# Kernel optimization log

Hardware: AMD Instinct MI355X
Metric: run time of the kernel (lower is better)

## Reference

```python
import jax, jax.numpy as jnp
import numpy as np

B, Q, K, H = 8, 512, 512, 1024
NH, HD = 16, 64
MAX_REL = 512  # max_relative_positions


def setup_inputs() -> dict:
    key = jax.random.key(0)
    ks = jax.random.split(key, 16)
    s = 1.0 / np.sqrt(H)
    inp = {
        "query": jax.random.normal(ks[0], (B, Q, H), jnp.float32),
        "key": jax.random.normal(ks[1], (B, K, H), jnp.float32),
        "value": jax.random.normal(ks[2], (B, K, H), jnp.float32),
        "key_padding_mask": jax.random.randint(ks[3], (B, K), 0, 2, jnp.int32),
        "Wq": jax.random.normal(ks[4], (H, H), jnp.float32) * s,
        "bq": jnp.zeros((H,), jnp.float32),
        "Wk": jax.random.normal(ks[5], (H, H), jnp.float32) * s,
        "bk": jnp.zeros((H,), jnp.float32),
        "Wv": jax.random.normal(ks[6], (H, H), jnp.float32) * s,
        "bv": jnp.zeros((H,), jnp.float32),
        "Wo": jax.random.normal(ks[7], (H, H), jnp.float32) * s,
        "bo": jnp.zeros((H,), jnp.float32),
        "rel_table": jax.random.normal(ks[8], (2 * MAX_REL - 1, NH), jnp.float32) * 0.02,
        "local_bias": jax.random.normal(ks[9], (512, 512), jnp.float32) * 0.1,
        "log_scale": jnp.zeros((1,), jnp.float32),
        "attention_bias": jnp.zeros((1,), jnp.float32),
    }
    return inp


def reference(query, key, value, key_padding_mask, Wq, bq, Wk, bk, Wv, bv, Wo, bo,
              rel_table, local_bias, log_scale, attention_bias):
    # projections -> [B, NH, len, HD]
    q = (query @ Wq + bq).reshape(B, Q, NH, HD).transpose(0, 2, 1, 3)
    k = (key @ Wk + bk).reshape(B, K, NH, HD).transpose(0, 2, 1, 3)
    v = (value @ Wv + bv).reshape(B, K, NH, HD).transpose(0, 2, 1, 3)

    scores = jnp.einsum('bhqd,bhkd->bhqk', q, k) / jnp.sqrt(jnp.float32(HD))

    # relative position bias
    rel = jnp.arange(Q)[:, None] - jnp.arange(K)[None, :]
    bucket = jnp.clip(rel, -(MAX_REL - 1), MAX_REL - 1) + (MAX_REL - 1)
    rel_bias = rel_table[bucket]            # [Q, K, NH]
    scores = scores + rel_bias.transpose(2, 0, 1)[None]  # [1, NH, Q, K]

    # local bias (Q,K <= 512)
    scores = scores + local_bias[:Q, :K][None, None] * 0.05

    scale = jnp.clip(jnp.exp(log_scale), 1.0, 4.0)
    scores = scores * scale + attention_bias

    pad = (key_padding_mask == 0)[:, None, None, :]  # [B,1,1,K]
    scores = jnp.where(pad, -jnp.inf, scores)
    # clamp AFTER masking: -inf -> -50 (padded keys get tiny but nonzero weight)
    scores = jnp.clip(scores, -50.0, 50.0)

    attn = jax.nn.softmax(scores, axis=-1)
    out = jnp.einsum('bhqk,bhkd->bhqd', attn, v)
    out = out.transpose(0, 2, 1, 3).reshape(B, Q, H)
    out = out @ Wo + bo
    return out, attn
```

## Files before the change

### kernel.cpp

```cpp
#include <hip/hip_runtime.h>

#define B_ 8
#define LQ 512
#define LK 512
#define HDIM 1024
#define NH_ 16
#define HD_ 64

typedef unsigned short u16;
typedef __attribute__((ext_vector_type(4))) float f32x4;
typedef __attribute__((ext_vector_type(4))) int i32x4;
typedef __attribute__((ext_vector_type(8))) __bf16 bf16x8;

static __device__ __forceinline__ u16 f2bf(float f) {
    union { float f; unsigned u; } v; v.f = f;
    unsigned u = v.u;
    return (u16)((u + 0x7fffu + ((u >> 16) & 1u)) >> 16);
}

static __device__ __forceinline__ void gload_lds16(const u16* g, u16* l) {
    __builtin_amdgcn_global_load_lds((const __attribute__((address_space(1))) unsigned*)g,
                                     (__attribute__((address_space(3))) unsigned*)l, 16, 0, 0);
}

__global__ __launch_bounds__(256) void xcast_kernel(
    const float* __restrict__ x0, const float* __restrict__ x1, const float* __restrict__ x2,
    u16* __restrict__ o0, u16* __restrict__ o1, u16* __restrict__ o2)
{
    const float* X; u16* O;
    switch (blockIdx.z) { case 0: X = x0; O = o0; break; case 1: X = x1; O = o1; break;
                          default: X = x2; O = o2; }
    int i = blockIdx.x * 256 + threadIdx.x;
    f32x4 v = ((const f32x4*)X)[i];
    union { u16 u[4]; unsigned long long ull; } p;
    p.u[0] = f2bf(v[0]); p.u[1] = f2bf(v[1]); p.u[2] = f2bf(v[2]); p.u[3] = f2bf(v[3]);
    ((unsigned long long*)O)[i] = p.ull;
}

__global__ void wcast_kernel(const float* __restrict__ w0, const float* __restrict__ w1,
                             const float* __restrict__ w2, const float* __restrict__ w3,
                             u16* __restrict__ o0, u16* __restrict__ o1,
                             u16* __restrict__ o2, u16* __restrict__ o3) {
    const float* W; u16* O;
    switch (blockIdx.z) { case 0: W = w0; O = o0; break; case 1: W = w1; O = o1; break;
                          case 2: W = w2; O = o2; break; default: W = w3; O = o3; }
    __shared__ float t[32][33];
    int tx = threadIdx.x, ty = threadIdx.y;
    int n0 = blockIdx.x * 32, k0 = blockIdx.y * 32;
#pragma unroll
    for (int i = 0; i < 4; i++) {
        int k = ty * 4 + i;
        t[k][tx] = W[(k0 + k) * HDIM + n0 + tx];
    }
    __syncthreads();
#pragma unroll
    for (int i = 0; i < 4; i++) {
        int n = ty * 4 + i;
        O[(n0 + n) * HDIM + k0 + tx] = f2bf(t[tx][n]);
    }
}

__global__ __launch_bounds__(256) void proj2_kernel(
    const u16* __restrict__ x0, const u16* __restrict__ x1, const u16* __restrict__ x2,
    const u16* __restrict__ wt0, const u16* __restrict__ wt1, const u16* __restrict__ wt2,
    const float* __restrict__ bi0, const float* __restrict__ bi1, const float* __restrict__ bi2,
    u16* __restrict__ ot0, u16* __restrict__ ot1, u16* __restrict__ ot2)
{
    __shared__ u16 As[128 * 64];
    __shared__ u16 Bs[128 * 64];
    int bid = blockIdx.x;
    int swz = (bid & 7) * 96 + (bid >> 3);
    int z = swz >> 8, rem = swz & 255;
    int Mb = (rem >> 3) * 128, Nb = (rem & 7) * 128;
    const u16* X; const u16* WT; const float* bias; u16* out;
    switch (z) {
        case 0: X = x0; WT = wt0; bias = bi0; out = ot0; break;
        case 1: X = x1; WT = wt1; bias = bi1; out = ot1; break;
        default: X = x2; WT = wt2; bias = bi2; out = ot2; break;
    }
    int tid = threadIdx.x, lane = tid & 63, w = tid >> 6;
    int wm = (w & 1) * 64, wn = (w >> 1) * 64;
    int r16 = lane & 15, kg = lane >> 4;
    int rsw = (r16 & 7) * 8;
    int srow = lane >> 3;
    int scol = 8 * ((lane & 7) ^ (lane >> 3));
    const u16* gA = X + (size_t)Mb * HDIM;
    const u16* gB = WT + (size_t)Nb * HDIM;

    f32x4 acc[4][4] = {};
    for (int k0 = 0; k0 < HDIM; k0 += 64) {
#pragma unroll
        for (int i = 0; i < 4; i++) {
            int c = w * 4 + i;
            int row = c * 8 + srow;
            gload_lds16(&gA[(size_t)row * HDIM + k0 + scol], &As[c * 512]);
            gload_lds16(&gB[(size_t)row * HDIM + k0 + scol], &Bs[c * 512]);
        }
        __syncthreads();
#pragma unroll
        for (int kk = 0; kk < 2; kk++) {
            int colp = (kk * 32 + kg * 8) ^ rsw;
            bf16x8 a[4], b[4];
#pragma unroll
            for (int mt = 0; mt < 4; mt++) a[mt] = *(const bf16x8*)&As[(wm + mt * 16 + r16) * 64 + colp];
#pragma unroll
            for (int nt = 0; nt < 4; nt++) b[nt] = *(const bf16x8*)&Bs[(wn + nt * 16 + r16) * 64 + colp];
#pragma unroll
            for (int mt = 0; mt < 4; mt++)
#pragma unroll
                for (int nt = 0; nt < 4; nt++)
                    acc[mt][nt] = __builtin_amdgcn_mfma_f32_16x16x32_bf16(a[mt], b[nt], acc[mt][nt], 0, 0, 0);
        }
        __syncthreads();
    }
    int cr = (lane >> 4) * 4, cc = lane & 15;
#pragma unroll
    for (int nt = 0; nt < 4; nt++) {
        int n = Nb + wn + nt * 16 + cc;
        float bv = bias[n];
        int h = n >> 6, d = n & 63;
#pragma unroll
        for (int mt = 0; mt < 4; mt++) {
#pragma unroll
            for (int j = 0; j < 4; j++) {
                int m = Mb + wm + mt * 16 + cr + j;
                int b = m >> 9, l = m & 511;
                out[(((b * NH_ + h) * LQ) + l) * HD_ + d] = f2bf(acc[mt][nt][j] + bv);
            }
        }
    }
}

__global__ void vtrans_kernel(const u16* __restrict__ vb, u16* __restrict__ vT) {
    int bh = blockIdx.z;
    int k0 = blockIdx.x * 32, d0 = blockIdx.y * 32;
    __shared__ u16 t[32][33];
    int tx = threadIdx.x, ty = threadIdx.y;
    const u16* src = vb + (size_t)bh * (LK * HD_);
    u16* dst = vT + (size_t)bh * (LK * HD_);
#pragma unroll
    for (int i = 0; i < 4; i++) {
        int k = ty * 4 + i;
        t[k][tx] = src[(k0 + k) * HD_ + d0 + tx];
    }
    __syncthreads();
#pragma unroll
    for (int i = 0; i < 4; i++) {
        int d = ty * 4 + i;
        dst[(d0 + d) * LK + k0 + tx] = t[tx][d];
    }
}

__global__ __launch_bounds__(512) void scores_kernel(
    const u16* __restrict__ qb, const u16* __restrict__ kb,
    const int* __restrict__ kpm, const float* __restrict__ rel_table,
    const float* __restrict__ local_bias, const float* __restrict__ log_scale,
    const float* __restrict__ att_bias, float* __restrict__ attn_out)
{
    __shared__ u16 Qs[32][72];
    __shared__ float rel_l[1024];
    __shared__ int pmask[512];
    __shared__ float red[2][32][8];

    int bh = blockIdx.y;
    int q0 = blockIdx.x * 32;
    int b = bh >> 4, h = bh & 15;
    int tid = threadIdx.x, lane = tid & 63, w = tid >> 6;
    int r16 = lane & 15, kg = lane >> 4;

    float scale = fminf(fmaxf(__expf(log_scale[0]), 1.0f), 4.0f);
    float abias = att_bias[0];

    if (tid < 256) {
        int row = tid >> 3, c8 = tid & 7;
        *(i32x4*)&Qs[row][c8 * 8] = *(const i32x4*)&qb[((size_t)bh * LQ + q0 + row) * HD_ + c8 * 8];
    }
    for (int i = tid; i < 1023; i += 512) rel_l[i] = rel_table[i * NH_ + h];
    pmask[tid & 511] = kpm[b * LK + (tid & 511)];
    __syncthreads();

    bf16x8 aq[2][2];
#pragma unroll
    for (int m = 0; m < 2; m++)
#pragma unroll
        for (int kk = 0; kk < 2; kk++)
            aq[m][kk] = *(const bf16x8*)&Qs[m * 16 + r16][kk * 32 + kg * 8];

    f32x4 acc[2][4] = {};
    const u16* kbase = kb + ((size_t)bh * LK + w * 64) * HD_;
#pragma unroll
    for (int nt = 0; nt < 4; nt++) {
        bf16x8 bk0 = *(const bf16x8*)&kbase[(nt * 16 + r16) * HD_ + kg * 8];
        bf16x8 bk1 = *(const bf16x8*)&kbase[(nt * 16 + r16) * HD_ + 32 + kg * 8];
#pragma unroll
        for (int m = 0; m < 2; m++) {
            acc[m][nt] = __builtin_amdgcn_mfma_f32_16x16x32_bf16(aq[m][0], bk0, acc[m][nt], 0, 0, 0);
            acc[m][nt] = __builtin_amdgcn_mfma_f32_16x16x32_bf16(aq[m][1], bk1, acc[m][nt], 0, 0, 0);
        }
    }

    float rm[2][4];
#pragma unroll
    for (int m = 0; m < 2; m++)
#pragma unroll
        for (int j = 0; j < 4; j++) rm[m][j] = -1e30f;
#pragma unroll
    for (int m = 0; m < 2; m++) {
#pragma unroll
        for (int nt = 0; nt < 4; nt++) {
            int ki = w * 64 + nt * 16 + r16;
            bool masked = (pmask[ki] == 0);
#pragma unroll
            for (int j = 0; j < 4; j++) {
                int row = m * 16 + kg * 4 + j;
                int qi = q0 + row;
                float s = acc[m][nt][j] * 0.125f;
                s += rel_l[qi - ki + 511];
                s += local_bias[qi * LK + ki] * 0.05f;
                s = s * scale + abias;
                s = masked ? -50.0f : fminf(fmaxf(s, -50.0f), 50.0f);
                acc[m][nt][j] = s;
                rm[m][j] = fmaxf(rm[m][j], s);
            }
        }
    }
#pragma unroll
    for (int m = 0; m < 2; m++)
#pragma unroll
        for (int j = 0; j < 4; j++) {
            float v = rm[m][j];
            v = fmaxf(v, __shfl_xor(v, 1));
            v = fmaxf(v, __shfl_xor(v, 2));
            v = fmaxf(v, __shfl_xor(v, 4));
            v = fmaxf(v, __shfl_xor(v, 8));
            rm[m][j] = v;
        }
    if (r16 == 0) {
#pragma unroll
        for (int m = 0; m < 2; m++)
#pragma unroll
            for (int j = 0; j < 4; j++) red[0][m * 16 + kg * 4 + j][w] = rm[m][j];
    }
    __syncthreads();
    float fm[2][4];
#pragma unroll
    for (int m = 0; m < 2; m++)
#pragma unroll
        for (int j = 0; j < 4; j++) {
            int row = m * 16 + kg * 4 + j;
            float v = red[0][row][0];
#pragma unroll
            for (int ww = 1; ww < 8; ww++) v = fmaxf(v, red[0][row][ww]);
            fm[m][j] = v;
        }
    float ps[2][4] = {};
#pragma unroll
    for (int m = 0; m < 2; m++)
#pragma unroll
        for (int nt = 0; nt < 4; nt++)
#pragma unroll
            for (int j = 0; j < 4; j++) {
                float e = __expf(acc[m][nt][j] - fm[m][j]);
                acc[m][nt][j] = e;
                ps[m][j] += e;
            }
#pragma unroll
    for (int m = 0; m < 2; m++)
#pragma unroll
        for (int j = 0; j < 4; j++) {
            float v = ps[m][j];
            v += __shfl_xor(v, 1);
            v += __shfl_xor(v, 2);
            v += __shfl_xor(v, 4);
            v += __shfl_xor(v, 8);
            ps[m][j] = v;
        }
    if (r16 == 0) {
#pragma unroll
        for (int m = 0; m < 2; m++)
#pragma unroll
            for (int j = 0; j < 4; j++) red[1][m * 16 + kg * 4 + j][w] = ps[m][j];
    }
    __syncthreads();
    float* dst = attn_out + ((size_t)bh * LQ + q0) * (size_t)LK + w * 64;
#pragma unroll
    for (int m = 0; m < 2; m++)
#pragma unroll
        for (int j = 0; j < 4; j++) {
            int row = m * 16 + kg * 4 + j;
            float sum = 0.f;
#pragma unroll
            for (int ww = 0; ww < 8; ww++) sum += red[1][row][ww];
            float inv = 1.0f / sum;
#pragma unroll
            for (int nt = 0; nt < 4; nt++)
                dst[(size_t)row * LK + nt * 16 + r16] = acc[m][nt][j] * inv;
        }
}

__global__ __launch_bounds__(256) void pv_kernel(
    const float* __restrict__ attn, const u16* __restrict__ vT, u16* __restrict__ ctx)
{
    __shared__ u16 As[128][72];
    __shared__ u16 Bs[64][72];
    int bh = blockIdx.y;
    int b = bh >> 4, h = bh & 15;
    int Mb = blockIdx.x * 128;
    int tid = threadIdx.x, lane = tid & 63, wid = tid >> 6;
    int wm = wid >> 1, wn = wid & 1;
    int r16 = lane & 15, kg = lane >> 4;
    f32x4 acc[4][2] = {};
    const float* abase = attn + ((size_t)bh * LQ + Mb) * (size_t)LK;
    const u16* vbase = vT + (size_t)bh * (HD_ * LK);
    for (int kt = 0; kt < 8; kt++) {
#pragma unroll
        for (int i = 0; i < 8; i++) {
            int g = tid + i * 256;
            int row = g >> 4, c4 = g & 15;
            f32x4 av = *(const f32x4*)&abase[(size_t)row * LK + kt * 64 + c4 * 4];
            union { u16 u[4]; unsigned long long ull; } p;
            p.u[0] = f2bf(av[0]); p.u[1] = f2bf(av[1]);
            p.u[2] = f2bf(av[2]); p.u[3] = f2bf(av[3]);
            *(unsigned long long*)&As[row][c4 * 4] = p.ull;
        }
#pragma unroll
        for (int i = 0; i < 2; i++) {
            int g = tid + i * 256;
            int row = g >> 3, c8 = g & 7;
            *(i32x4*)&Bs[row][c8 * 8] = *(const i32x4*)&vbase[(size_t)row * LK + kt * 64 + c8 * 8];
        }
        __syncthreads();
#pragma unroll
        for (int kk = 0; kk < 2; kk++) {
            bf16x8 a[4], bfr[2];
#pragma unroll
            for (int mt = 0; mt < 4; mt++) a[mt] = *(const bf16x8*)&As[wm * 64 + mt * 16 + r16][kk * 32 + kg * 8];
#pragma unroll
            for (int nt = 0; nt < 2; nt++) bfr[nt] = *(const bf16x8*)&Bs[wn * 32 + nt * 16 + r16][kk * 32 + kg * 8];
#pragma unroll
            for (int mt = 0; mt < 4; mt++)
#pragma unroll
                for (int nt = 0; nt < 2; nt++)
                    acc[mt][nt] = __builtin_amdgcn_mfma_f32_16x16x32_bf16(a[mt], bfr[nt], acc[mt][nt], 0, 0, 0);
        }
        __syncthreads();
    }
    int cr = (lane >> 4) * 4, cc = lane & 15;
#pragma unroll
    for (int mt = 0; mt < 4; mt++) {
#pragma unroll
        for (int nt = 0; nt < 2; nt++) {
            int d = wn * 32 + nt * 16 + cc;
#pragma unroll
            for (int j = 0; j < 4; j++) {
                int q = Mb + wm * 64 + mt * 16 + cr + j;
                ctx[((size_t)(b * LQ + q)) * HDIM + h * HD_ + d] = f2bf(acc[mt][nt][j]);
            }
        }
    }
}

__global__ __launch_bounds__(256) void oproj2_kernel(
    const u16* __restrict__ ctx, const u16* __restrict__ WT,
    const float* __restrict__ bias, float* __restrict__ out)
{
    __shared__ u16 As[128 * 64];
    __shared__ u16 Bs[128 * 64];
    int bid = blockIdx.x;
    int idx = (bid & 7) * 32 + (bid >> 3);
    int Mb = (idx >> 3) * 128, Nb = (idx & 7) * 128;
    int tid = threadIdx.x, lane = tid & 63, w = tid >> 6;
    int wm = (w & 1) * 64, wn = (w >> 1) * 64;
    int r16 = lane & 15, kg = lane >> 4;
    int rsw = (r16 & 7) * 8;
    int srow = lane >> 3;
    int scol = 8 * ((lane & 7) ^ (lane >> 3));
    const u16* gA = ctx + (size_t)Mb * HDIM;
    const u16* gB = WT + (size_t)Nb * HDIM;

    f32x4 acc[4][4] = {};
    for (int k0 = 0; k0 < HDIM; k0 += 64) {
#pragma unroll
        for (int i = 0; i < 4; i++) {
            int c = w * 4 + i;
            int row = c * 8 + srow;
            gload_lds16(&gA[(size_t)row * HDIM + k0 + scol], &As[c * 512]);
            gload_lds16(&gB[(size_t)row * HDIM + k0 + scol], &Bs[c * 512]);
        }
        __syncthreads();
#pragma unroll
        for (int kk = 0; kk < 2; kk++) {
            int colp = (kk * 32 + kg * 8) ^ rsw;
            bf16x8 a[4], b[4];
#pragma unroll
            for (int mt = 0; mt < 4; mt++) a[mt] = *(const bf16x8*)&As[(wm + mt * 16 + r16) * 64 + colp];
#pragma unroll
            for (int nt = 0; nt < 4; nt++) b[nt] = *(const bf16x8*)&Bs[(wn + nt * 16 + r16) * 64 + colp];
#pragma unroll
            for (int mt = 0; mt < 4; mt++)
#pragma unroll
                for (int nt = 0; nt < 4; nt++)
                    acc[mt][nt] = __builtin_amdgcn_mfma_f32_16x16x32_bf16(a[mt], b[nt], acc[mt][nt], 0, 0, 0);
        }
        __syncthreads();
    }
    int cr = (lane >> 4) * 4, cc = lane & 15;
#pragma unroll
    for (int nt = 0; nt < 4; nt++) {
        int n = Nb + wn + nt * 16 + cc;
        float bv = bias[n];
#pragma unroll
        for (int mt = 0; mt < 4; mt++) {
#pragma unroll
            for (int j = 0; j < 4; j++) {
                int m = Mb + wm + mt * 16 + cr + j;
                out[(size_t)m * HDIM + n] = acc[mt][nt][j] + bv;
            }
        }
    }
}

extern "C" void kernel_launch(void* const* d_in, const int* in_sizes, int n_in,
                              void* d_out, int out_size, void* d_ws, size_t ws_size,
                              hipStream_t stream) {
    (void)in_sizes; (void)n_in; (void)out_size; (void)ws_size;
    const float* query = (const float*)d_in[0];
    const float* key_  = (const float*)d_in[1];
    const float* value = (const float*)d_in[2];
    const int*   kpm   = (const int*)d_in[3];
    const float* Wq = (const float*)d_in[4];  const float* bq = (const float*)d_in[5];
    const float* Wk = (const float*)d_in[6];  const float* bk = (const float*)d_in[7];
    const float* Wv = (const float*)d_in[8];  const float* bv = (const float*)d_in[9];
    const float* Wo = (const float*)d_in[10]; const float* bo = (const float*)d_in[11];
    const float* rel_table  = (const float*)d_in[12];
    const float* local_bias = (const float*)d_in[13];
    const float* log_scale  = (const float*)d_in[14];
    const float* att_bias   = (const float*)d_in[15];

    char* ws = (char*)d_ws;
    u16* WTq = (u16*)(ws + 0ull);
    u16* WTk = (u16*)(ws + (2ull << 20));
    u16* WTv = (u16*)(ws + (4ull << 20));
    u16* WTo = (u16*)(ws + (6ull << 20));
    u16* qb  = (u16*)(ws + (8ull << 20));
    u16* kb  = (u16*)(ws + (16ull << 20));
    u16* vb  = (u16*)(ws + (24ull << 20));
    u16* vT  = (u16*)(ws + (32ull << 20));
    u16* ctx = (u16*)(ws + (40ull << 20));
    u16* xq  = (u16*)(ws + (32ull << 20));
    u16* xk  = (u16*)(ws + (40ull << 20));
    u16* xv  = (u16*)(ws + (48ull << 20));

    float* out  = (float*)d_out;
    float* attn = out + (size_t)4096 * 1024;

    xcast_kernel<<<dim3(4096, 1, 3), 256, 0, stream>>>(query, key_, value, xq, xk, xv);
    wcast_kernel<<<dim3(32, 32, 4), dim3(32, 8), 0, stream>>>(Wq, Wk, Wv, Wo, WTq, WTk, WTv, WTo);
    proj2_kernel<<<768, 256, 0, stream>>>(xq, xk, xv, WTq, WTk, WTv, bq, bk, bv, qb, kb, vb);
    vtrans_kernel<<<dim3(16, 2, 128), dim3(32, 8), 0, stream>>>(vb, vT);
    scores_kernel<<<dim3(16, 128), 512, 0, stream>>>(qb, kb, kpm, rel_table, local_bias,
                                                     log_scale, att_bias, attn);
    pv_kernel<<<dim3(4, 128), 256, 0, stream>>>(attn, vT, ctx);
    oproj2_kernel<<<256, 256, 0, stream>>>(ctx, WTo, bo, out);
}
```

Measured before the change: 196.9 us.

## Fuse P·V into scores kernel using bf16 probabilities kept in LDS

Merges the separate pv_kernel into the scores/softmax kernel. Normalized probabilities are written to the fp32 attn output and also stored as bf16 in shared memory, then multiplied by V directly (V fragments read from global), with the two K-halves split across warps and reduced through LDS. This removes re-reading the 64 MB fp32 attention matrix and a kernel launch. The cost is about 36 KB of extra LDS per block, which may lower occupancy, and uncached global V fragment loads per warp.

```diff
diff --git a/kernel.cpp b/kernel.cpp
--- a/kernel.cpp
+++ b/kernel.cpp
@@ -151,16 +151,18 @@
     }
 }
 
-__global__ __launch_bounds__(512) void scores_kernel(
-    const u16* __restrict__ qb, const u16* __restrict__ kb,
+__global__ __launch_bounds__(512) void attn2_kernel(
+    const u16* __restrict__ qb, const u16* __restrict__ kb, const u16* __restrict__ vT,
     const int* __restrict__ kpm, const float* __restrict__ rel_table,
     const float* __restrict__ local_bias, const float* __restrict__ log_scale,
-    const float* __restrict__ att_bias, float* __restrict__ attn_out)
+    const float* __restrict__ att_bias, float* __restrict__ attn_out, u16* __restrict__ ctx)
 {
     __shared__ u16 Qs[32][72];
     __shared__ float rel_l[1024];
     __shared__ int pmask[512];
     __shared__ float red[2][32][8];
+    __shared__ u16 P[32][520];
+    __shared__ float pred[4][32][16];
 
     int bh = blockIdx.y;
     int q0 = blockIdx.x * 32;
@@ -282,6 +284,7 @@
             for (int j = 0; j < 4; j++) red[1][m * 16 + kg * 4 + j][w] = ps[m][j];
     }
     __syncthreads();
+
     float* dst = attn_out + ((size_t)bh * LQ + q0) * (size_t)LK + w * 64;
 #pragma unroll
     for (int m = 0; m < 2; m++)
@@ -293,70 +296,45 @@
             for (int ww = 0; ww < 8; ww++) sum += red[1][row][ww];
             float inv = 1.0f / sum;
 #pragma unroll
-            for (int nt = 0; nt < 4; nt++)
-                dst[(size_t)row * LK + nt * 16 + r16] = acc[m][nt][j] * inv;
-        }
-}
-
-__global__ __launch_bounds__(256) void pv_kernel(
-    const float* __restrict__ attn, const u16* __restrict__ vT, u16* __restrict__ ctx)
-{
-    __shared__ u16 As[128][72];
-    __shared__ u16 Bs[64][72];
-    int bh = blockIdx.y;
-    int b = bh >> 4, h = bh & 15;
-    int Mb = blockIdx.x * 128;
-    int tid = threadIdx.x, lane = tid & 63, wid = tid >> 6;
-    int wm = wid >> 1, wn = wid & 1;
-    int r16 = lane & 15, kg = lane >> 4;
-    f32x4 acc[4][2] = {};
-    const float* abase = attn + ((size_t)bh * LQ + Mb) * (size_t)LK;
+            for (int nt = 0; nt < 4; nt++) {
+                float p = acc[m][nt][j] * inv;
+                dst[(size_t)row * LK + nt * 16 + r16] = p;
+                P[row][w * 64 + nt * 16 + r16] = f2bf(p);
+            }
+        }
+    __syncthreads();
+
+    int wd = (w & 3) * 16;
+    int kh = (w >> 2) * 256;
     const u16* vbase = vT + (size_t)bh * (HD_ * LK);
+    f32x4 po[2] = {};
+#pragma unroll
     for (int kt = 0; kt < 8; kt++) {
-#pragma unroll
-        for (int i = 0; i < 8; i++) {
-            int g = tid + i * 256;
-            int row = g >> 4, c4 = g & 15;
-            f32x4 av = *(const f32x4*)&abase[(size_t)row * LK + kt * 64 + c4 * 4];
-            union { u16 u[4]; unsigned long long ull; } p;
-            p.u[0] = f2bf(av[0]); p.u[1] = f2bf(av[1]);
-            p.u[2] = f2bf(av[2]); p.u[3] = f2bf(av[3]);
-            *(unsigned long long*)&As[row][c4 * 4] = p.ull;
-        }
-#pragma unroll
-        for (int i = 0; i < 2; i++) {
-            int g = tid + i * 256;
-            int row = g >> 3, c8 = g & 7;
-            *(i32x4*)&Bs[row][c8 * 8] = *(const i32x4*)&vbase[(size_t)row * LK + kt * 64 + c8 * 8];
-        }
-        __syncthreads();
-#pragma unroll
-        for (int kk = 0; kk < 2; kk++) {
-            bf16x8 a[4], bfr[2];
-#pragma unroll
-            for (int mt = 0; mt < 4; mt++) a[mt] = *(const bf16x8*)&As[wm * 64 + mt * 16 + r16][kk * 32 + kg * 8];
-#pragma unroll
-            for (int nt = 0; nt < 2; nt++) bfr[nt] = *(const bf16x8*)&Bs[wn * 32 + nt * 16 + r16][kk * 32 + kg * 8];
-#pragma unroll
-            for (int mt = 0; mt < 4; mt++)
-#pragma unroll
-                for (int nt = 0; nt < 2; nt++)
-                    acc[mt][nt] = __builtin_amdgcn_mfma_f32_16x16x32_bf16(a[mt], bfr[nt], acc[mt][nt], 0, 0, 0);
-        }
-        __syncthreads();
-    }
-    int cr = (lane >> 4) * 4, cc = lane & 15;
-#pragma unroll
-    for (int mt = 0; mt < 4; mt++) {
-#pragma unroll
-        for (int nt = 0; nt < 2; nt++) {
-            int d = wn * 32 + nt * 16 + cc;
+        int k0 = kh + kt * 32;
+        bf16x8 bvf = *(const bf16x8*)&vbase[(size_t)(wd + r16) * LK + k0 + kg * 8];
+#pragma unroll
+        for (int m = 0; m < 2; m++) {
+            bf16x8 af = *(const bf16x8*)&P[m * 16 + r16][k0 + kg * 8];
+            po[m] = __builtin_amdgcn_mfma_f32_16x16x32_bf16(af, bvf, po[m], 0, 0, 0);
+        }
+    }
+    if (w >= 4) {
+#pragma unroll
+        for (int m = 0; m < 2; m++)
+#pragma unroll
+            for (int j = 0; j < 4; j++)
+                pred[w & 3][m * 16 + kg * 4 + j][r16] = po[m][j];
+    }
+    __syncthreads();
+    if (w < 4) {
+#pragma unroll
+        for (int m = 0; m < 2; m++)
 #pragma unroll
             for (int j = 0; j < 4; j++) {
-                int q = Mb + wm * 64 + mt * 16 + cr + j;
-                ctx[((size_t)(b * LQ + q)) * HDIM + h * HD_ + d] = f2bf(acc[mt][nt][j]);
-            }
-        }
+                int row = m * 16 + kg * 4 + j;
+                float v = po[m][j] + pred[w][row][r16];
+                ctx[((size_t)(b * LQ + q0 + row)) * HDIM + h * HD_ + wd + r16] = f2bf(v);
+            }
     }
 }
 
@@ -458,8 +436,7 @@
     wcast_kernel<<<dim3(32, 32, 4), dim3(32, 8), 0, stream>>>(Wq, Wk, Wv, Wo, WTq, WTk, WTv, WTo);
     proj2_kernel<<<768, 256, 0, stream>>>(xq, xk, xv, WTq, WTk, WTv, bq, bk, bv, qb, kb, vb);
     vtrans_kernel<<<dim3(16, 2, 128), dim3(32, 8), 0, stream>>>(vb, vT);
-    scores_kernel<<<dim3(16, 128), 512, 0, stream>>>(qb, kb, kpm, rel_table, local_bias,
-                                                     log_scale, att_bias, attn);
-    pv_kernel<<<dim3(4, 128), 256, 0, stream>>>(attn, vT, ctx);
+    attn2_kernel<<<dim3(16, 128), 512, 0, stream>>>(qb, kb, vT, kpm, rel_table, local_bias,
+                                                    log_scale, att_bias, attn, ctx);
     oproj2_kernel<<<256, 256, 0, stream>>>(ctx, WTo, bo, out);
 }
```

Measured after the change: 182.2 us. 7.5% less time.
